# Performance work log

Hardware: AMD Instinct MI355X
Metric: run time of the kernel (lower is better)

## Reference

```python
import jax, jax.numpy as jnp
import numpy as np

FRAME_LEN, HOP, FFT_LEN = 400, 160, 512
PREEMPH = 0.97
MEL_FLOOR = 1.192092955078125e-07


def _hz_to_mel(f):
    return 2595.0 * np.log10(1.0 + f / 700.0)


def _build_mel_filters():
    # mirrors mel_filter_bank(256, 80, 20, 8000, 16000) with filter_freqs = mel_freqs (as in source)
    num_freq_bins, num_mel = 256, 80
    mel_min, mel_max = _hz_to_mel(20.0), _hz_to_mel(8000.0)
    filter_freqs = np.linspace(mel_min, mel_max, num_mel + 2)
    fft_bin_width = 16000.0 / (num_freq_bins * 2)
    fft_freqs = _hz_to_mel(fft_bin_width * np.arange(num_freq_bins))
    filter_diff = np.diff(filter_freqs)
    slopes = filter_freqs[None, :] - fft_freqs[:, None]  # (256, 82)
    down = -slopes[:, :-2] / filter_diff[:-1]
    up = slopes[:, 2:] / filter_diff[1:]
    fb = np.maximum(0.0, np.minimum(down, up))  # (256, 80)
    return np.pad(fb, ((0, 1), (0, 0))).astype(np.float32)  # (257, 80)


def _build_window():
    n = np.arange(FRAME_LEN)
    hann = 0.5 * (1.0 - np.cos(2.0 * np.pi * n / (FRAME_LEN - 1)))  # periodic=False
    return (hann ** 0.85).astype(np.float32)


def setup_inputs() -> dict:
    key = jax.random.key(0)
    k1, = jax.random.split(key, 1)
    B, N = 32, 480000
    raw_speech = jax.random.normal(k1, (B, N), dtype=jnp.float32)
    mask = jnp.ones((B, N), dtype=jnp.float32)
    return {
        "raw_speech": raw_speech,
        "mask": mask,
        "mel_filters": jnp.asarray(_build_mel_filters()),
        "window": jnp.asarray(_build_window()),
    }


def reference(raw_speech, mask, mel_filters, window):
    stride, pad_mult, padding_value = 2, 2, 1.0
    wav = raw_speech * 32768.0  # * 2**15
    B, N = wav.shape
    num_frames = 1 + (N - FRAME_LEN) // HOP
    # vectorized framing (replaces per-frame python loop)
    idx = jnp.arange(num_frames)[:, None] * HOP + jnp.arange(FRAME_LEN)[None, :]
    frames = wav[:, idx]      # (B, F, 400)
    mframes = mask[:, idx]    # (B, F, 400)
    # remove DC offset
    frames = frames - frames.mean(axis=-1, keepdims=True)
    # preemphasis (first sample scaled by 1-p, matching the source)
    frames = jnp.concatenate(
        [frames[..., :1] * (1.0 - PREEMPH), frames[..., 1:] - PREEMPH * frames[..., :-1]],
        axis=-1,
    )
    frames = frames * window * mframes
    spec = jnp.fft.rfft(frames, n=FFT_LEN, axis=-1)  # (B, F, 257) zero-padded fft
    power = jnp.abs(spec) ** 2.0
    feats = jnp.log(jnp.maximum(power @ mel_filters, MEL_FLOOR))  # (B, F, 80)
    # per-utterance normalization over frames (unbiased variance)
    mean = feats.mean(axis=1, keepdims=True)
    var = feats.var(axis=1, keepdims=True, ddof=1)
    feats = (feats - mean) / jnp.sqrt(var + 1e-7)
    # stride-stacking
    rem = num_frames % stride
    F2 = num_frames - rem
    feats = feats[:, :F2].reshape(B, F2 // stride, 80 * stride)
    # pad frames dim to multiple of pad_to_multiple_of with padding_value
    n = feats.shape[1]
    P = (pad_mult - n % pad_mult) % pad_mult
    input_features = jnp.pad(feats, ((0, 0), (0, P), (0, 0)), constant_values=padding_value)
    attention_mask = jnp.concatenate(
        [jnp.ones((B, n), jnp.int32), jnp.zeros((B, P), jnp.int32)], axis=1
    )
    return input_features, attention_mask
```

## Files before the change

kernel.cpp:

```cpp
#include <hip/hip_runtime.h>
#include <math.h>

#define NFRAMES 2998
#define BATCH 32
#define NSAMP 480000
#define NMEL 80
#define NBINS 257
#define ROWS 1500
#define COLS 160
#define MEL_FLOOR 1.192092955078125e-07f
#define PI_F 3.14159265358979323846f
#define SCHUNKS 32

#define SW(a) ((a) ^ ((a) >> 5))

template<int NS>
__device__ inline void r4pass(const float* __restrict__ sre, const float* __restrict__ sim,
                              float* __restrict__ dre, float* __restrict__ dim_, int j)
{
    const int k = j & (NS - 1);
    float ar = sre[SW(j)],       ai = sim[SW(j)];
    float br = sre[SW(j + 64)],  bi = sim[SW(j + 64)];
    float cr = sre[SW(j + 128)], ci = sim[SW(j + 128)];
    float dr = sre[SW(j + 192)], di = sim[SW(j + 192)];

    float t1r, t1i, t2r, t2i, t3r, t3i;
    if (NS == 1) {
        t1r = br; t1i = bi; t2r = cr; t2i = ci; t3r = dr; t3i = di;
    } else {
        float s1, c1;
        __sincosf((-PI_F / (2.0f * (float)NS)) * (float)k, &s1, &c1);
        float c2 = c1 * c1 - s1 * s1, s2 = 2.0f * c1 * s1;
        float c3 = c1 * c2 - s1 * s2, s3 = c1 * s2 + s1 * c2;
        t1r = br * c1 - bi * s1; t1i = br * s1 + bi * c1;
        t2r = cr * c2 - ci * s2; t2i = cr * s2 + ci * c2;
        t3r = dr * c3 - di * s3; t3i = dr * s3 + di * c3;
    }
    float e0r = ar + t2r,  e0i = ai + t2i;
    float e1r = ar - t2r,  e1i = ai - t2i;
    float e2r = t1r + t3r, e2i = t1i + t3i;
    float e3r = t1r - t3r, e3i = t1i - t3i;
    const int i0 = 4 * j - 3 * k;
    dre[SW(i0)]          = e0r + e2r;  dim_[SW(i0)]          = e0i + e2i;
    dre[SW(i0 + NS)]     = e1r + e3i;  dim_[SW(i0 + NS)]     = e1i - e3r;
    dre[SW(i0 + 2*NS)]   = e0r - e2r;  dim_[SW(i0 + 2*NS)]   = e0i - e2i;
    dre[SW(i0 + 3*NS)]   = e1r - e3i;  dim_[SW(i0 + 3*NS)]   = e1i + e3r;
}

__global__ __launch_bounds__(256) void k_ranges(const float* __restrict__ fil,
                                                int* __restrict__ rlo, int* __restrict__ rlen)
{
    const int m    = blockIdx.x * 4 + (threadIdx.x >> 6);
    const int lane = threadIdx.x & 63;
    int lo = NBINS, hi = -1;
    for (int f = lane; f < NBINS; f += 64) {
        if (fil[f * NMEL + m] > 0.f) { lo = min(lo, f); hi = max(hi, f); }
    }
    #pragma unroll
    for (int o = 1; o < 64; o <<= 1) {
        lo = min(lo, __shfl_xor(lo, o, 64));
        hi = max(hi, __shfl_xor(hi, o, 64));
    }
    if (lane == 0) {
        rlo[m]  = (hi < 0) ? 0 : lo;
        rlen[m] = (hi < 0) ? 0 : (hi - lo + 1);
    }
}

__global__ __launch_bounds__(256) void k_frames(
    const float* __restrict__ raw, const float* __restrict__ mask,
    const float* __restrict__ fil, const float* __restrict__ win,
    const int* __restrict__ rlo, const int* __restrict__ rlen,
    float* __restrict__ feats)
{
    __shared__ float Are[4][256];
    __shared__ float Aim[4][256];
    __shared__ __align__(16) union {
        struct { float x[896]; float mk[896]; } in;
        struct { float re[4][256]; float im[4][256]; } c;
    } U;
    __shared__ float s_pow[4][NBINS];

    const int tid  = threadIdx.x;
    const int wv   = tid >> 6;
    const int lane = tid & 63;
    const int b    = blockIdx.y;
    const int fr0  = blockIdx.x * 4;
    const long sbase = (long)b * NSAMP + (long)fr0 * 160;
    const int  valid = NSAMP - fr0 * 160;

    for (int i4 = tid; i4 < 220; i4 += 256) {
        float4 xv = make_float4(0.f, 0.f, 0.f, 0.f);
        float4 mv = make_float4(0.f, 0.f, 0.f, 0.f);
        if (i4 * 4 + 4 <= valid) {
            xv = *(const float4*)(raw  + sbase + i4 * 4);
            mv = *(const float4*)(mask + sbase + i4 * 4);
        }
        xv.x *= 32768.f; xv.y *= 32768.f; xv.z *= 32768.f; xv.w *= 32768.f;
        *(float4*)&U.in.x[i4 * 4]  = xv;
        *(float4*)&U.in.mk[i4 * 4] = mv;
    }
    __syncthreads();

    float part = 0.f;
    for (int i = lane; i < 400; i += 64) part += U.in.x[wv * 160 + i];
    #pragma unroll
    for (int o = 1; o < 64; o <<= 1) part += __shfl_xor(part, o, 64);
    const float fmean = part * (1.0f / 400.0f);

    {
        const int l = lane;
        float ys[8];
        if (l < 50) {
            const float* xp = &U.in.x[wv * 160 + 8 * l];
            const float* mp = &U.in.mk[wv * 160 + 8 * l];
            float4 x0 = *(const float4*)xp,        x1 = *(const float4*)(xp + 4);
            float4 m0 = *(const float4*)mp,        m1 = *(const float4*)(mp + 4);
            float4 w0 = *(const float4*)(win + 8 * l), w1 = *(const float4*)(win + 8 * l + 4);
            float xm1 = (l > 0) ? xp[-1] : 0.f;
            float xs[8] = {x0.x, x0.y, x0.z, x0.w, x1.x, x1.y, x1.z, x1.w};
            float ms[8] = {m0.x, m0.y, m0.z, m0.w, m1.x, m1.y, m1.z, m1.w};
            float wf[8] = {w0.x, w0.y, w0.z, w0.w, w1.x, w1.y, w1.z, w1.w};
            #pragma unroll
            for (int e = 0; e < 8; ++e) {
                float xc = xs[e];
                float xprev = e ? xs[e - 1] : xm1;
                float y = (8 * l + e == 0) ? 0.03f * (xc - fmean)
                                           : (xc - 0.97f * xprev - 0.03f * fmean);
                ys[e] = y * wf[e] * ms[e];
            }
        } else {
            #pragma unroll
            for (int e = 0; e < 8; ++e) ys[e] = 0.f;
        }
        __syncthreads();
        #pragma unroll
        for (int d = 0; d < 4; ++d) {
            Are[wv][SW(4 * l + d)] = ys[2 * d];
            Aim[wv][SW(4 * l + d)] = ys[2 * d + 1];
        }
    }

    r4pass<1 >(&Are[wv][0], &Aim[wv][0], &U.c.re[wv][0], &U.c.im[wv][0], lane);
    r4pass<4 >(&U.c.re[wv][0], &U.c.im[wv][0], &Are[wv][0], &Aim[wv][0], lane);
    r4pass<16>(&Are[wv][0], &Aim[wv][0], &U.c.re[wv][0], &U.c.im[wv][0], lane);
    r4pass<64>(&U.c.re[wv][0], &U.c.im[wv][0], &Are[wv][0], &Aim[wv][0], lane);

    #pragma unroll
    for (int q = 0; q < 4; ++q) {
        int k  = lane + 64 * q;
        int a  = k & 255;
        int b2 = (256 - k) & 255;
        float zar = Are[wv][SW(a)],  zai = Aim[wv][SW(a)];
        float zbr = Are[wv][SW(b2)], zbi = Aim[wv][SW(b2)];
        float Er  = 0.5f * (zar + zbr), Ei = 0.5f * (zai - zbi);
        float Or_ = 0.5f * (zai + zbi), Oi = 0.5f * (zbr - zar);
        float sk, ck;
        __sincosf((-PI_F / 256.0f) * (float)k, &sk, &ck);
        float Xr = Er + ck * Or_ - sk * Oi;
        float Xi = Ei + ck * Oi + sk * Or_;
        s_pow[wv][k] = Xr * Xr + Xi * Xi;
    }
    if (lane == 0) {
        float zr = Are[wv][SW(0)], zi = Aim[wv][SW(0)];
        float Xr = zr - zi;
        s_pow[wv][256] = Xr * Xr;
    }
    __syncthreads();

    for (int p = tid; p < 4 * NMEL; p += 256) {
        int g = p / NMEL, m = p - NMEL * g;
        int fr = fr0 + g;
        if (fr >= NFRAMES) continue;
        int lo = rlo[m], len = rlen[m];
        float acc = 0.f;
        for (int i = 0; i < len; ++i) {
            int f = lo + i;
            acc = fmaf(s_pow[g][f], fil[f * NMEL + m], acc);
        }
        feats[((long)b * NFRAMES + fr) * NMEL + m] = __logf(fmaxf(acc, MEL_FLOOR));
    }
}

__global__ __launch_bounds__(256) void k_stats1(const float* __restrict__ feats,
                                                float* __restrict__ partials)
{
    const int b  = blockIdx.x;
    const int ch = blockIdx.y;
    const int t  = threadIdx.x;
    const int fr0 = (NFRAMES * ch) / SCHUNKS;
    const int fr1 = (NFRAMES * (ch + 1)) / SCHUNKS;

    float4 s  = make_float4(0.f, 0.f, 0.f, 0.f);
    float4 s2 = make_float4(0.f, 0.f, 0.f, 0.f);
    if (t < 240) {
        const int c = t % 20;
        const int r = t / 20;
        const float4* base = (const float4*)(feats + (long)b * NFRAMES * NMEL);
        for (int fr = fr0 + r; fr < fr1; fr += 12) {
            float4 v = base[(long)fr * 20 + c];
            s.x += v.x; s.y += v.y; s.z += v.z; s.w += v.w;
            s2.x += v.x * v.x; s2.y += v.y * v.y; s2.z += v.z * v.z; s2.w += v.w * v.w;
        }
    }
    __shared__ float4 ls[240], ls2[240];
    if (t < 240) { ls[t] = s; ls2[t] = s2; }
    __syncthreads();
    if (t < 20) {
        float4 a = ls[t], a2 = ls2[t];
        for (int r = 1; r < 12; ++r) {
            float4 u = ls[r * 20 + t], u2 = ls2[r * 20 + t];
            a.x += u.x; a.y += u.y; a.z += u.z; a.w += u.w;
            a2.x += u2.x; a2.y += u2.y; a2.z += u2.z; a2.w += u2.w;
        }
        float4* p = (float4*)(partials + (long)(b * SCHUNKS + ch) * 2 * NMEL);
        p[t]      = a;
        p[20 + t] = a2;
    }
}

__global__ __launch_bounds__(128) void k_stats2(const float* __restrict__ partials,
                                                float* __restrict__ meanv,
                                                float* __restrict__ rstdv)
{
    const int b = blockIdx.x;
    const int m = threadIdx.x;
    if (m >= NMEL) return;
    float s = 0.f, s2 = 0.f;
    for (int ch = 0; ch < SCHUNKS; ++ch) {
        const float* p = partials + (long)(b * SCHUNKS + ch) * 2 * NMEL;
        s  += p[m];
        s2 += p[NMEL + m];
    }
    float mean = s * (1.0f / NFRAMES);
    float var  = (s2 - s * s * (1.0f / NFRAMES)) * (1.0f / (NFRAMES - 1));
    meanv[b * NMEL + m] = mean;
    rstdv[b * NMEL + m] = rsqrtf(var + 1e-7f);
}

__global__ __launch_bounds__(256) void k_out(const float* __restrict__ feats,
                                             const float* __restrict__ meanv,
                                             const float* __restrict__ rstdv,
                                             float* __restrict__ out)
{
    const int totf4 = BATCH * ROWS * COLS / 4;
    const int totm  = BATCH * ROWS;
    const int idx = blockIdx.x * blockDim.x + threadIdx.x;
    const int stride = gridDim.x * blockDim.x;

    for (int i = idx; i < totf4; i += stride) {
        int e = i * 4;
        int b  = e / (ROWS * COLS);
        int rc = e % (ROWS * COLS);
        int r = rc / COLS, c = rc % COLS;
        float4 o;
        if (r == ROWS - 1) {
            o = make_float4(1.f, 1.f, 1.f, 1.f);
        } else {
            int fr = 2 * r + (c >= NMEL);
            int m  = c % NMEL;
            const float4 f  = *(const float4*)(feats + ((long)b * NFRAMES + fr) * NMEL + m);
            const float4 mu = *(const float4*)(meanv + b * NMEL + m);
            const float4 rs = *(const float4*)(rstdv + b * NMEL + m);
            o.x = (f.x - mu.x) * rs.x;
            o.y = (f.y - mu.y) * rs.y;
            o.z = (f.z - mu.z) * rs.z;
            o.w = (f.w - mu.w) * rs.w;
        }
        *(float4*)(out + e) = o;
    }

    float* omask = out + (long)BATCH * ROWS * COLS;
    for (int i = idx; i < totm; i += stride) {
        int r = i % ROWS;
        omask[i] = (r == ROWS - 1) ? 0.0f : 1.0f;
    }
}

extern "C" void kernel_launch(void* const* d_in, const int* in_sizes, int n_in,
                              void* d_out, int out_size, void* d_ws, size_t ws_size,
                              hipStream_t stream)
{
    const float* raw  = (const float*)d_in[0];
    const float* mask = (const float*)d_in[1];
    const float* fil  = (const float*)d_in[2];
    const float* win  = (const float*)d_in[3];
    float* out = (float*)d_out;

    float* feats    = (float*)d_ws;
    float* meanv    = feats + (long)BATCH * NFRAMES * NMEL;
    float* rstdv    = meanv + BATCH * NMEL;
    float* partials = rstdv + BATCH * NMEL;
    int*   rlo      = (int*)(partials + (long)BATCH * SCHUNKS * 2 * NMEL);
    int*   rlen     = rlo + NMEL;

    k_ranges<<<20, 256, 0, stream>>>(fil, rlo, rlen);

    dim3 g1((NFRAMES + 3) / 4, BATCH);
    k_frames<<<g1, 256, 0, stream>>>(raw, mask, fil, win, rlo, rlen, feats);

    dim3 gs(BATCH, SCHUNKS);
    k_stats1<<<gs, 256, 0, stream>>>(feats, partials);
    k_stats2<<<BATCH, 128, 0, stream>>>(partials, meanv, rstdv);

    k_out<<<2048, 256, 0, stream>>>(feats, meanv, rstdv, out);
}
```

Baseline: 274.4 us.

## Interleave FFT scratch as float2 and fuse stats finalization into output kernel

The FFT scratch buffers change from separate real and imaginary arrays to interleaved float2 with a new XOR swizzle, so each complex element is read or written with one 64-bit LDS access. The k_stats2 kernel is removed: each k_out block reduces the per-chunk partial sums for its batch into shared-memory mean and rstd. k_out now runs on a (16, batch) grid. This drops one launch and the mean/rstd round trip through global memory. The cost is that all 16 blocks per batch redo the small reduction, and the new swizzle may cause bank conflicts.

```diff
diff --git a/kernel.cpp b/kernel.cpp
--- a/kernel.cpp
+++ b/kernel.cpp
@@ -12,39 +12,38 @@
 #define PI_F 3.14159265358979323846f
 #define SCHUNKS 32
 
-#define SW(a) ((a) ^ ((a) >> 5))
+#define SW2(a) ((a) ^ (5 * (((a) >> 4) & 3)))
 
 template<int NS>
-__device__ inline void r4pass(const float* __restrict__ sre, const float* __restrict__ sim,
-                              float* __restrict__ dre, float* __restrict__ dim_, int j)
+__device__ inline void r4pass2(const float2* __restrict__ s, float2* __restrict__ d, int j)
 {
     const int k = j & (NS - 1);
-    float ar = sre[SW(j)],       ai = sim[SW(j)];
-    float br = sre[SW(j + 64)],  bi = sim[SW(j + 64)];
-    float cr = sre[SW(j + 128)], ci = sim[SW(j + 128)];
-    float dr = sre[SW(j + 192)], di = sim[SW(j + 192)];
+    float2 va = s[SW2(j)];
+    float2 vb = s[SW2(j + 64)];
+    float2 vc = s[SW2(j + 128)];
+    float2 vd = s[SW2(j + 192)];
 
     float t1r, t1i, t2r, t2i, t3r, t3i;
     if (NS == 1) {
-        t1r = br; t1i = bi; t2r = cr; t2i = ci; t3r = dr; t3i = di;
+        t1r = vb.x; t1i = vb.y; t2r = vc.x; t2i = vc.y; t3r = vd.x; t3i = vd.y;
     } else {
         float s1, c1;
         __sincosf((-PI_F / (2.0f * (float)NS)) * (float)k, &s1, &c1);
         float c2 = c1 * c1 - s1 * s1, s2 = 2.0f * c1 * s1;
         float c3 = c1 * c2 - s1 * s2, s3 = c1 * s2 + s1 * c2;
-        t1r = br * c1 - bi * s1; t1i = br * s1 + bi * c1;
-        t2r = cr * c2 - ci * s2; t2i = cr * s2 + ci * c2;
-        t3r = dr * c3 - di * s3; t3i = dr * s3 + di * c3;
-    }
-    float e0r = ar + t2r,  e0i = ai + t2i;
-    float e1r = ar - t2r,  e1i = ai - t2i;
-    float e2r = t1r + t3r, e2i = t1i + t3i;
-    float e3r = t1r - t3r, e3i = t1i - t3i;
+        t1r = vb.x * c1 - vb.y * s1; t1i = vb.x * s1 + vb.y * c1;
+        t2r = vc.x * c2 - vc.y * s2; t2i = vc.x * s2 + vc.y * c2;
+        t3r = vd.x * c3 - vd.y * s3; t3i = vd.x * s3 + vd.y * c3;
+    }
+    float e0r = va.x + t2r, e0i = va.y + t2i;
+    float e1r = va.x - t2r, e1i = va.y - t2i;
+    float e2r = t1r + t3r,  e2i = t1i + t3i;
+    float e3r = t1r - t3r,  e3i = t1i - t3i;
     const int i0 = 4 * j - 3 * k;
-    dre[SW(i0)]          = e0r + e2r;  dim_[SW(i0)]          = e0i + e2i;
-    dre[SW(i0 + NS)]     = e1r + e3i;  dim_[SW(i0 + NS)]     = e1i - e3r;
-    dre[SW(i0 + 2*NS)]   = e0r - e2r;  dim_[SW(i0 + 2*NS)]   = e0i - e2i;
-    dre[SW(i0 + 3*NS)]   = e1r - e3i;  dim_[SW(i0 + 3*NS)]   = e1i + e3r;
+    d[SW2(i0)]          = make_float2(e0r + e2r, e0i + e2i);
+    d[SW2(i0 + NS)]     = make_float2(e1r + e3i, e1i - e3r);
+    d[SW2(i0 + 2*NS)]   = make_float2(e0r - e2r, e0i - e2i);
+    d[SW2(i0 + 3*NS)]   = make_float2(e1r - e3i, e1i + e3r);
 }
 
 __global__ __launch_bounds__(256) void k_ranges(const float* __restrict__ fil,
@@ -73,11 +72,10 @@
     const int* __restrict__ rlo, const int* __restrict__ rlen,
     float* __restrict__ feats)
 {
-    __shared__ float Are[4][256];
-    __shared__ float Aim[4][256];
+    __shared__ float2 A2[4][256];
     __shared__ __align__(16) union {
         struct { float x[896]; float mk[896]; } in;
-        struct { float re[4][256]; float im[4][256]; } c;
+        float2 c2[4][256];
     } U;
     __shared__ float s_pow[4][NBINS];
 
@@ -136,25 +134,24 @@
         __syncthreads();
         #pragma unroll
         for (int d = 0; d < 4; ++d) {
-            Are[wv][SW(4 * l + d)] = ys[2 * d];
-            Aim[wv][SW(4 * l + d)] = ys[2 * d + 1];
-        }
-    }
-
-    r4pass<1 >(&Are[wv][0], &Aim[wv][0], &U.c.re[wv][0], &U.c.im[wv][0], lane);
-    r4pass<4 >(&U.c.re[wv][0], &U.c.im[wv][0], &Are[wv][0], &Aim[wv][0], lane);
-    r4pass<16>(&Are[wv][0], &Aim[wv][0], &U.c.re[wv][0], &U.c.im[wv][0], lane);
-    r4pass<64>(&U.c.re[wv][0], &U.c.im[wv][0], &Are[wv][0], &Aim[wv][0], lane);
+            A2[wv][SW2(4 * l + d)] = make_float2(ys[2 * d], ys[2 * d + 1]);
+        }
+    }
+
+    r4pass2<1 >(&A2[wv][0],   &U.c2[wv][0], lane);
+    r4pass2<4 >(&U.c2[wv][0], &A2[wv][0],   lane);
+    r4pass2<16>(&A2[wv][0],   &U.c2[wv][0], lane);
+    r4pass2<64>(&U.c2[wv][0], &A2[wv][0],   lane);
 
     #pragma unroll
     for (int q = 0; q < 4; ++q) {
         int k  = lane + 64 * q;
         int a  = k & 255;
         int b2 = (256 - k) & 255;
-        float zar = Are[wv][SW(a)],  zai = Aim[wv][SW(a)];
-        float zbr = Are[wv][SW(b2)], zbi = Aim[wv][SW(b2)];
-        float Er  = 0.5f * (zar + zbr), Ei = 0.5f * (zai - zbi);
-        float Or_ = 0.5f * (zai + zbi), Oi = 0.5f * (zbr - zar);
+        float2 za = A2[wv][SW2(a)];
+        float2 zb = A2[wv][SW2(b2)];
+        float Er  = 0.5f * (za.x + zb.x), Ei = 0.5f * (za.y - zb.y);
+        float Or_ = 0.5f * (za.y + zb.y), Oi = 0.5f * (zb.x - za.x);
         float sk, ck;
         __sincosf((-PI_F / 256.0f) * (float)k, &sk, &ck);
         float Xr = Er + ck * Or_ - sk * Oi;
@@ -162,8 +159,8 @@
         s_pow[wv][k] = Xr * Xr + Xi * Xi;
     }
     if (lane == 0) {
-        float zr = Are[wv][SW(0)], zi = Aim[wv][SW(0)];
-        float Xr = zr - zi;
+        float2 z0 = A2[wv][SW2(0)];
+        float Xr = z0.x - z0.y;
         s_pow[wv][256] = Xr * Xr;
     }
     __syncthreads();
@@ -219,61 +216,54 @@
     }
 }
 
-__global__ __launch_bounds__(128) void k_stats2(const float* __restrict__ partials,
-                                                float* __restrict__ meanv,
-                                                float* __restrict__ rstdv)
-{
-    const int b = blockIdx.x;
-    const int m = threadIdx.x;
-    if (m >= NMEL) return;
-    float s = 0.f, s2 = 0.f;
-    for (int ch = 0; ch < SCHUNKS; ++ch) {
-        const float* p = partials + (long)(b * SCHUNKS + ch) * 2 * NMEL;
-        s  += p[m];
-        s2 += p[NMEL + m];
-    }
-    float mean = s * (1.0f / NFRAMES);
-    float var  = (s2 - s * s * (1.0f / NFRAMES)) * (1.0f / (NFRAMES - 1));
-    meanv[b * NMEL + m] = mean;
-    rstdv[b * NMEL + m] = rsqrtf(var + 1e-7f);
-}
-
 __global__ __launch_bounds__(256) void k_out(const float* __restrict__ feats,
-                                             const float* __restrict__ meanv,
-                                             const float* __restrict__ rstdv,
+                                             const float* __restrict__ partials,
                                              float* __restrict__ out)
 {
-    const int totf4 = BATCH * ROWS * COLS / 4;
-    const int totm  = BATCH * ROWS;
-    const int idx = blockIdx.x * blockDim.x + threadIdx.x;
-    const int stride = gridDim.x * blockDim.x;
-
-    for (int i = idx; i < totf4; i += stride) {
+    const int b = blockIdx.y;
+    const int t = threadIdx.x;
+    __shared__ float sm[NMEL], sr[NMEL];
+
+    if (t < NMEL) {
+        const float* p = partials + (long)b * SCHUNKS * 2 * NMEL;
+        float s = 0.f, s2 = 0.f;
+        #pragma unroll 4
+        for (int ch = 0; ch < SCHUNKS; ++ch) {
+            s  += p[ch * 2 * NMEL + t];
+            s2 += p[ch * 2 * NMEL + NMEL + t];
+        }
+        float mean = s * (1.0f / NFRAMES);
+        float var  = (s2 - s * s * (1.0f / NFRAMES)) * (1.0f / (NFRAMES - 1));
+        sm[t] = mean;
+        sr[t] = rsqrtf(var + 1e-7f);
+    }
+    __syncthreads();
+
+    const int tot4 = ROWS * COLS / 4;
+    float* ob = out + (long)b * ROWS * COLS;
+    for (int i = blockIdx.x * 256 + t; i < tot4; i += gridDim.x * 256) {
         int e = i * 4;
-        int b  = e / (ROWS * COLS);
-        int rc = e % (ROWS * COLS);
-        int r = rc / COLS, c = rc % COLS;
+        int r = e / COLS, c = e % COLS;
         float4 o;
         if (r == ROWS - 1) {
             o = make_float4(1.f, 1.f, 1.f, 1.f);
         } else {
             int fr = 2 * r + (c >= NMEL);
             int m  = c % NMEL;
-            const float4 f  = *(const float4*)(feats + ((long)b * NFRAMES + fr) * NMEL + m);
-            const float4 mu = *(const float4*)(meanv + b * NMEL + m);
-            const float4 rs = *(const float4*)(rstdv + b * NMEL + m);
-            o.x = (f.x - mu.x) * rs.x;
-            o.y = (f.y - mu.y) * rs.y;
-            o.z = (f.z - mu.z) * rs.z;
-            o.w = (f.w - mu.w) * rs.w;
-        }
-        *(float4*)(out + e) = o;
-    }
-
-    float* omask = out + (long)BATCH * ROWS * COLS;
-    for (int i = idx; i < totm; i += stride) {
-        int r = i % ROWS;
-        omask[i] = (r == ROWS - 1) ? 0.0f : 1.0f;
+            const float4 f = *(const float4*)(feats + ((long)b * NFRAMES + fr) * NMEL + m);
+            o.x = (f.x - sm[m])     * sr[m];
+            o.y = (f.y - sm[m + 1]) * sr[m + 1];
+            o.z = (f.z - sm[m + 2]) * sr[m + 2];
+            o.w = (f.w - sm[m + 3]) * sr[m + 3];
+        }
+        *(float4*)(ob + e) = o;
+    }
+
+    if (blockIdx.x == 0) {
+        float* omask = out + (long)BATCH * ROWS * COLS + (long)b * ROWS;
+        for (int i = t; i < ROWS; i += 256) {
+            omask[i] = (i == ROWS - 1) ? 0.0f : 1.0f;
+        }
     }
 }
 
@@ -288,9 +278,7 @@
     float* out = (float*)d_out;
 
     float* feats    = (float*)d_ws;
-    float* meanv    = feats + (long)BATCH * NFRAMES * NMEL;
-    float* rstdv    = meanv + BATCH * NMEL;
-    float* partials = rstdv + BATCH * NMEL;
+    float* partials = feats + (long)BATCH * NFRAMES * NMEL;
     int*   rlo      = (int*)(partials + (long)BATCH * SCHUNKS * 2 * NMEL);
     int*   rlen     = rlo + NMEL;
 
@@ -301,7 +289,7 @@
 
     dim3 gs(BATCH, SCHUNKS);
     k_stats1<<<gs, 256, 0, stream>>>(feats, partials);
-    k_stats2<<<BATCH, 128, 0, stream>>>(partials, meanv, rstdv);
-
-    k_out<<<2048, 256, 0, stream>>>(feats, meanv, rstdv, out);
-}
+
+    dim3 go(16, BATCH);
+    k_out<<<go, 256, 0, stream>>>(feats, partials, out);
+}
```

New measurement: 273.3 us. No clear change (-0.4%).
